# Performance work log

Hardware: AMD Instinct MI355X
Metric: run time of the kernel (lower is better)

## Reference

```python
import jax, jax.numpy as jnp
import numpy as np

H = 2        # num_heads
C = 128      # in_channels
K_ORDER = 4
BETA = 0.5


def _gcn_conv(x, row, col, deg_inv, n):
    # x: [N, H, C]; adj_t = D^{-1} A^T where A[row, col] = 1
    # (adj_t @ x)[c] = deg_inv[c] * sum_{e: col_e == c} x[row_e]
    msg = x[row]  # [E, H, C]
    agg = jax.ops.segment_sum(msg, col, num_segments=n)  # [N, H, C]
    return agg * deg_inv[:, None, None]


def _attn_conv(qs, ks, vs):
    # linear (kernelized) attention, non-block path
    n = qs.shape[0]
    kvs = jnp.einsum('lhm,lhd->hmd', ks, vs)            # [H, C, C]
    qkvs = jnp.einsum('nhm,hmd->nhd', qs, kvs)          # [N, H, C]
    vs_sum = vs.sum(axis=0)                             # [H, C]
    num = qkvs + vs_sum[None, :, :]
    ks_sum = ks.sum(axis=0)                             # [H, C]
    qks_sum = jnp.einsum('nhm,hm->nh', qs, ks_sum)[:, :, None]  # [N, H, 1]
    den = qks_sum + jnp.asarray(n, qs.dtype)
    return num / den


def setup_inputs() -> dict:
    key = jax.random.key(0)
    ks = jax.random.split(key, 8)
    N, E = 100000, 1600000
    x = jax.random.normal(ks[0], (N, C), jnp.float32)
    edge_index = jax.random.randint(ks[1], (2, E), 0, N, jnp.int64)
    s_in = 1.0 / np.sqrt(C)
    s_out = 1.0 / np.sqrt(H * C * (K_ORDER + 1))
    Wq_w = jax.random.normal(ks[2], (C, H * C), jnp.float32) * s_in
    Wq_b = jax.random.normal(ks[3], (H * C,), jnp.float32) * s_in
    Wk_w = jax.random.normal(ks[4], (C, H * C), jnp.float32) * s_in
    Wk_b = jax.random.normal(ks[5], (H * C,), jnp.float32) * s_in
    Wo_w = jax.random.normal(ks[6], (H * C * (K_ORDER + 1), C), jnp.float32) * s_out
    Wo_b = jax.random.normal(ks[7], (C,), jnp.float32) * s_out
    return {"x": x, "edge_index": edge_index, "Wq_w": Wq_w, "Wq_b": Wq_b,
            "Wk_w": Wk_w, "Wk_b": Wk_b, "Wo_w": Wo_w, "Wo_b": Wo_b}


def reference(x, edge_index, Wq_w, Wq_b, Wk_w, Wk_b, Wo_w, Wo_b):
    n = x.shape[0]
    row, col = edge_index[0], edge_index[1]
    # normalized adjacency D^{-1} A^T (pow(-1.0) in the source, not -0.5)
    deg = jax.ops.segment_sum(jnp.ones(row.shape[0], x.dtype), col, num_segments=n)
    deg_inv = jnp.where(deg > 0, 1.0 / deg, 0.0)

    query = (x @ Wq_w + Wq_b).reshape(n, H, C)
    key = (x @ Wk_w + Wk_b).reshape(n, H, C)
    qs = query / jnp.linalg.norm(query, axis=2, keepdims=True)
    ks = key / jnp.linalg.norm(key, axis=2, keepdims=True)

    x0 = jnp.broadcast_to(x[:, None, :], (n, H, C))  # [N, H, C]
    terms = [x0]
    for _ in range(K_ORDER):
        prev = terms[-1]
        gcn_i = _gcn_conv(prev, row, col, deg_inv, n)
        attn_i = _attn_conv(qs, ks, prev)
        terms.append(BETA * gcn_i + attn_i)
    xcat = jnp.concatenate(terms, axis=-1)  # [N, H, C*(K+1)]
    xcat = xcat.reshape(n, H * C * (K_ORDER + 1))
    return (xcat @ Wo_w + Wo_b) / H
```

## Files before the change

### kernel.cpp

```cpp
#include <hip/hip_runtime.h>

#define THREADS 256
#define NB 512
#define SEGCAP 6144

typedef __attribute__((ext_vector_type(8))) short short8;
typedef __attribute__((ext_vector_type(4))) float f32x4;

__device__ __forceinline__ float bf2f(unsigned short u) {
    union { unsigned int i; float f; } v;
    v.i = ((unsigned int)u) << 16;
    return v.f;
}
__device__ __forceinline__ unsigned short f2bf(float f) {
    union { float f; unsigned int i; } v;
    v.f = f;
    unsigned int r = (v.i + 0x7FFFu + ((v.i >> 16) & 1u)) >> 16;
    return (unsigned short)r;
}
__device__ __forceinline__ float4 ld4f(const float* p) {
    return *reinterpret_cast<const float4*>(p);
}
__device__ __forceinline__ float4 ld4f(const unsigned short* p) {
    ushort4 u = *reinterpret_cast<const ushort4*>(p);
    return make_float4(bf2f(u.x), bf2f(u.y), bf2f(u.z), bf2f(u.w));
}

__device__ __forceinline__ int edge_get(const int* base, int E, int mode, int which, int e) {
    size_t idx = (size_t)which * (size_t)E + (size_t)e;
    return mode ? base[2 * idx] : base[idx];
}

__global__ __launch_bounds__(256) void k_detect(const int* __restrict__ e, int E,
                                                int* __restrict__ mode) {
    __shared__ int nz;
    if (threadIdx.x == 0) nz = 0;
    __syncthreads();
    int lim = 2 * E;
    if (lim > 8192) lim = 8192;
    for (int i = 1 + 2 * (int)threadIdx.x; i < lim; i += 512)
        if (e[i] != 0) nz = 1;
    __syncthreads();
    if (threadIdx.x == 0) *mode = (nz == 0) ? 1 : 0;
}

__global__ __launch_bounds__(256) void k_hist(const int* __restrict__ eb, int E,
                                              const int* __restrict__ mode, int N, int CW, int epb,
                                              int* __restrict__ gcnt) {
    __shared__ int hist[NB];
    for (int i = threadIdx.x; i < NB; i += 256) hist[i] = 0;
    __syncthreads();
    int m = *mode;
    int e0 = blockIdx.x * epb;
    int e1 = min(e0 + epb, E);
    for (int e = e0 + threadIdx.x; e < e1; e += 256) {
        int c = edge_get(eb, E, m, 1, e);
        if ((unsigned)c < (unsigned)N) atomicAdd(&hist[c / CW], 1);
    }
    __syncthreads();
    for (int i = threadIdx.x; i < NB; i += 256)
        if (hist[i]) atomicAdd(&gcnt[i], hist[i]);
}

__global__ __launch_bounds__(NB) void k_bscan(const int* __restrict__ gcnt,
                                              int* __restrict__ gbase, int* __restrict__ gcursor) {
    __shared__ int s[NB];
    int t = threadIdx.x;
    int v = gcnt[t];
    s[t] = v;
    __syncthreads();
    for (int off = 1; off < NB; off <<= 1) {
        int add = (t >= off) ? s[t - off] : 0;
        __syncthreads();
        s[t] += add;
        __syncthreads();
    }
    gbase[t] = s[t] - v;
    gcursor[t] = s[t] - v;
}

__global__ __launch_bounds__(256) void k_part(const int* __restrict__ eb, int E,
                                              const int* __restrict__ mode, int N, int CW, int epb,
                                              int* __restrict__ gcursor, uint2* __restrict__ ebuf) {
    __shared__ int hist[NB];
    __shared__ int base[NB];
    for (int i = threadIdx.x; i < NB; i += 256) hist[i] = 0;
    __syncthreads();
    int m = *mode;
    int e0 = blockIdx.x * epb;
    int e1 = min(e0 + epb, E);
    for (int e = e0 + threadIdx.x; e < e1; e += 256) {
        int c = edge_get(eb, E, m, 1, e);
        if ((unsigned)c < (unsigned)N) atomicAdd(&hist[c / CW], 1);
    }
    __syncthreads();
    for (int i = threadIdx.x; i < NB; i += 256) {
        int h = hist[i];
        base[i] = h ? atomicAdd(&gcursor[i], h) : 0;
        hist[i] = 0;
    }
    __syncthreads();
    for (int e = e0 + threadIdx.x; e < e1; e += 256) {
        int c = edge_get(eb, E, m, 1, e);
        if ((unsigned)c < (unsigned)N) {
            int r = edge_get(eb, E, m, 0, e);
            if ((unsigned)r >= (unsigned)N) r = 0;
            int b = c / CW;
            int li = atomicAdd(&hist[b], 1);
            ebuf[(size_t)base[b] + li] = make_uint2((unsigned)r, (unsigned)c);
        }
    }
}

__global__ __launch_bounds__(256) void k_build(const uint2* __restrict__ ebuf,
                                               const int* __restrict__ gbase,
                                               const int* __restrict__ gcnt, int N, int CW,
                                               int* __restrict__ cnt, int* __restrict__ offs,
                                               float* __restrict__ deg_inv, int* __restrict__ csr) {
    __shared__ int hist[256];
    __shared__ int pfx[256];
    __shared__ int seg[SEGCAP];
    const int b = blockIdx.x;
    const int col0 = b * CW;
    const int ncols = min(CW, N - col0);
    if (ncols <= 0) return;
    const int ebase = gbase[b], ecnt = gcnt[b];
    const int t = threadIdx.x;
    for (int i = t; i < 256; i += 256) hist[i] = 0;
    __syncthreads();
    for (int e = t; e < ecnt; e += 256) {
        uint2 rc = ebuf[(size_t)ebase + e];
        atomicAdd(&hist[rc.y - col0], 1);
    }
    __syncthreads();
    int v = (t < ncols) ? hist[t] : 0;
    pfx[t] = v;
    __syncthreads();
    for (int off = 1; off < 256; off <<= 1) {
        int add = (t >= off) ? pfx[t - off] : 0;
        __syncthreads();
        pfx[t] += add;
        __syncthreads();
    }
    int excl = pfx[t] - v;
    if (t < ncols) {
        cnt[col0 + t] = v;
        offs[col0 + t] = ebase + excl;
        deg_inv[col0 + t] = (v > 0) ? 1.0f / (float)v : 0.0f;
    }
    __syncthreads();
    if (t < 256) hist[t] = (t < ncols) ? excl : 0;
    __syncthreads();
    if (ecnt <= SEGCAP) {
        for (int e = t; e < ecnt; e += 256) {
            uint2 rc = ebuf[(size_t)ebase + e];
            int li = atomicAdd(&hist[rc.y - col0], 1);
            seg[li] = (int)rc.x;
        }
        __syncthreads();
        for (int e = t; e < ecnt; e += 256) csr[(size_t)ebase + e] = seg[e];
    } else {
        for (int e = t; e < ecnt; e += 256) {
            uint2 rc = ebuf[(size_t)ebase + e];
            int li = atomicAdd(&hist[rc.y - col0], 1);
            csr[(size_t)ebase + li] = (int)rc.x;
        }
    }
}

__global__ __launch_bounds__(256) void k_prep_wqk(const float* __restrict__ Wq,
                                                  const float* __restrict__ Wk,
                                                  unsigned short* __restrict__ WqkT) {
    int i = blockIdx.x * 256 + threadIdx.x;
    if (i < 512 * 128) {
        int oc = i >> 7, k = i & 127;
        float v = (oc < 256) ? Wq[k * 256 + oc] : Wk[k * 256 + (oc - 256)];
        WqkT[i] = f2bf(v);
    }
}

__global__ __launch_bounds__(256) void k_prep_wo(const float* __restrict__ Wo,
                                                 unsigned short* __restrict__ WoT) {
    int i = blockIdx.x * 256 + threadIdx.x;
    if (i < 1280 * 128) {
        int r = i >> 7, j = i & 127;
        WoT[(size_t)j * 1280 + r] = f2bf(Wo[i]);
    }
}

__global__ __launch_bounds__(256) void k_proj(const float* __restrict__ x,
                                              const unsigned short* __restrict__ WqkT,
                                              const float* __restrict__ bq,
                                              const float* __restrict__ bk,
                                              unsigned short* __restrict__ qs,
                                              unsigned short* __restrict__ ks, int N) {
    __shared__ unsigned short xs[64 * 128];
    __shared__ unsigned short os[64 * 256];
    const int t = threadIdx.x;
    const int n0 = blockIdx.x * 64;
#pragma unroll
    for (int i = 0; i < 4; i++) {
        int chunk = i * 256 + t;
        int r = chunk >> 4, c0 = (chunk & 15) * 8;
        float4 a0 = make_float4(0.f, 0.f, 0.f, 0.f), a1 = a0;
        if (n0 + r < N) {
            a0 = ld4f(&x[(size_t)(n0 + r) * 128 + c0]);
            a1 = ld4f(&x[(size_t)(n0 + r) * 128 + c0 + 4]);
        }
        short8 v = {(short)f2bf(a0.x), (short)f2bf(a0.y), (short)f2bf(a0.z), (short)f2bf(a0.w),
                    (short)f2bf(a1.x), (short)f2bf(a1.y), (short)f2bf(a1.z), (short)f2bf(a1.w)};
        int byte = r * 256 + ((c0 * 2) ^ ((r & 7) << 4));
        *reinterpret_cast<short8*>(reinterpret_cast<char*>(xs) + byte) = v;
    }
    __syncthreads();
    const int w = t >> 6, l = t & 63, lrow = l & 15, lhi = l >> 4;
    f32x4 acc[4][8];
    const f32x4 fz = {0.f, 0.f, 0.f, 0.f};
#pragma unroll
    for (int mt = 0; mt < 4; mt++)
#pragma unroll
        for (int nt = 0; nt < 8; nt++) acc[mt][nt] = fz;

    for (int kk = 0; kk < 4; kk++) {
        int kb = kk * 32 + lhi * 8;
        short8 af[4];
#pragma unroll
        for (int mt = 0; mt < 4; mt++) {
            int r = mt * 16 + lrow;
            af[mt] = *reinterpret_cast<const short8*>(
                reinterpret_cast<const char*>(xs) + r * 256 + ((kb * 2) ^ ((r & 7) << 4)));
        }
#pragma unroll
        for (int nt = 0; nt < 8; nt++) {
            int oc = w * 128 + nt * 16 + lrow;
            short8 bf = *reinterpret_cast<const short8*>(&WqkT[(size_t)oc * 128 + kb]);
#pragma unroll
            for (int mt = 0; mt < 4; mt++)
                acc[mt][nt] = __builtin_amdgcn_mfma_f32_16x16x32_bf16(af[mt], bf, acc[mt][nt], 0, 0, 0);
        }
    }
#pragma unroll
    for (int nt = 0; nt < 8; nt++) {
        int oc = w * 128 + nt * 16 + lrow;
        float b = (oc < 256) ? bq[oc] : bk[oc - 256];
#pragma unroll
        for (int mt = 0; mt < 4; mt++)
#pragma unroll
            for (int reg = 0; reg < 4; reg++) acc[mt][nt][reg] += b;
    }
    const int hc = (w & 1) * 128;
    float rv[4][4];
#pragma unroll
    for (int mt = 0; mt < 4; mt++) {
        float ss[4] = {0.f, 0.f, 0.f, 0.f};
#pragma unroll
        for (int nt = 0; nt < 8; nt++)
#pragma unroll
            for (int reg = 0; reg < 4; reg++) ss[reg] += acc[mt][nt][reg] * acc[mt][nt][reg];
#pragma unroll
        for (int m_ = 1; m_ < 16; m_ <<= 1)
#pragma unroll
            for (int reg = 0; reg < 4; reg++) ss[reg] += __shfl_xor(ss[reg], m_);
#pragma unroll
        for (int reg = 0; reg < 4; reg++) rv[mt][reg] = rsqrtf(ss[reg]);
    }
    for (int pass = 0; pass < 2; pass++) {
        if ((w >> 1) == pass) {
#pragma unroll
            for (int mt = 0; mt < 4; mt++)
#pragma unroll
                for (int reg = 0; reg < 4; reg++) {
                    int r = mt * 16 + lhi * 4 + reg;
#pragma unroll
                    for (int nt = 0; nt < 8; nt++)
                        os[r * 256 + hc + nt * 16 + lrow] = f2bf(acc[mt][nt][reg] * rv[mt][reg]);
                }
        }
        __syncthreads();
        unsigned short* dstg = pass ? ks : qs;
#pragma unroll
        for (int i = 0; i < 8; i++) {
            int chunk = i * 256 + t;
            int r = chunk >> 5, c = (chunk & 31) * 8;
            int n = n0 + r;
            if (n < N)
                *reinterpret_cast<short8*>(&dstg[(size_t)n * 256 + c]) =
                    *reinterpret_cast<const short8*>(&os[r * 256 + c]);
        }
        __syncthreads();
    }
}

__global__ __launch_bounds__(256) void k_colsum(const unsigned short* __restrict__ ks, int N,
                                                float* __restrict__ part) {
    const int t = threadIdx.x;
    const int stride = (N + 255) >> 8;
    int r0 = blockIdx.x * stride;
    int rend = min(r0 + stride, N);
    float s = 0.f;
    for (int n = r0; n < rend; n++) s += bf2f(ks[(size_t)n * 256 + t]);
    part[blockIdx.x * 256 + t] = s;
}

__global__ __launch_bounds__(256) void k_colsum2(const float* __restrict__ part,
                                                 float* __restrict__ ks_sum) {
    const int t = threadIdx.x;
    float s = 0.f;
    for (int b = 0; b < 256; b++) s += part[b * 256 + t];
    ks_sum[t] = s;
}

__global__ __launch_bounds__(256) void k_den(const unsigned short* __restrict__ qs,
                                             const float* __restrict__ ks_sum,
                                             float* __restrict__ den, int N) {
    int w = threadIdx.x >> 6, lane = threadIdx.x & 63;
    int n = blockIdx.x * 4 + w;
    if (n >= N) return;
    float4 q = ld4f(&qs[(size_t)n * 256 + lane * 4]);
    float4 kv = *reinterpret_cast<const float4*>(&ks_sum[lane * 4]);
    float s = q.x * kv.x + q.y * kv.y + q.z * kv.z + q.w * kv.w;
#pragma unroll
    for (int off = 1; off < 32; off <<= 1) s += __shfl_xor(s, off);
    if ((lane & 31) == 0) den[n * 2 + (lane >> 5)] = s + (float)N;
}

__device__ __forceinline__ short8 frag_ld(const unsigned short* tile, int kb, int col) {
    const char* b = reinterpret_cast<const char*>(tile);
    int cb = (col * 2) ^ (((kb >> 3) & 3) << 5);
    short8 r;
#pragma unroll
    for (int i = 0; i < 8; i++)
        r[i] = (short)*reinterpret_cast<const unsigned short*>(b + (kb + i) * 512 + cb);
    return r;
}

template <typename TV>
__global__ __launch_bounds__(256) void k_kvs2(const unsigned short* __restrict__ ks,
                                              const TV* __restrict__ vs, int vstride, int vmask,
                                              float* __restrict__ partial,
                                              float* __restrict__ pvsum, int rows_per, int N) {
    __shared__ unsigned short kt[32 * 256];
    __shared__ unsigned short vt[32 * 256];
    __shared__ float vred[8][256];
    const int t = threadIdx.x;
    const int w = t >> 6, l = t & 63, lrow = l & 15, lhi = l >> 4;
    const int h = w >> 1, mhalf = w & 1;
    const int r0 = blockIdx.x * rows_per;
    const int rend = min(r0 + rows_per, N);

    const f32x4 fz = {0.f, 0.f, 0.f, 0.f};
    f32x4 acc[4][8];
#pragma unroll
    for (int mt = 0; mt < 4; mt++)
#pragma unroll
        for (int nt = 0; nt < 8; nt++) acc[mt][nt] = fz;
    float vsum8[8] = {0.f, 0.f, 0.f, 0.f, 0.f, 0.f, 0.f, 0.f};

    for (int c0 = r0; c0 < rend; c0 += 32) {
#pragma unroll
        for (int i = 0; i < 4; i++) {
            int chunk = i * 256 + t;
            int n = chunk >> 5, cc = (chunk & 31) * 8;
            short8 v = {0, 0, 0, 0, 0, 0, 0, 0};
            if (c0 + n < rend)
                v = *reinterpret_cast<const short8*>(&ks[(size_t)(c0 + n) * 256 + cc]);
            *reinterpret_cast<short8*>(reinterpret_cast<char*>(kt) + n * 512 +
                                       ((cc * 2) ^ (((n >> 3) & 3) << 5))) = v;
        }
#pragma unroll
        for (int i = 0; i < 4; i++) {
            int chunk = i * 256 + t;
            int n = chunk >> 5, cc = (chunk & 31) * 8;
            float4 a0 = make_float4(0.f, 0.f, 0.f, 0.f), a1 = a0;
            if (c0 + n < rend) {
                a0 = ld4f(&vs[(size_t)(c0 + n) * vstride + (cc & vmask)]);
                a1 = ld4f(&vs[(size_t)(c0 + n) * vstride + ((cc + 4) & vmask)]);
            }
            unsigned short u0 = f2bf(a0.x), u1 = f2bf(a0.y), u2 = f2bf(a0.z), u3 = f2bf(a0.w);
            unsigned short u4 = f2bf(a1.x), u5 = f2bf(a1.y), u6 = f2bf(a1.z), u7 = f2bf(a1.w);
            vsum8[0] += bf2f(u0); vsum8[1] += bf2f(u1); vsum8[2] += bf2f(u2); vsum8[3] += bf2f(u3);
            vsum8[4] += bf2f(u4); vsum8[5] += bf2f(u5); vsum8[6] += bf2f(u6); vsum8[7] += bf2f(u7);
            short8 v = {(short)u0, (short)u1, (short)u2, (short)u3,
                        (short)u4, (short)u5, (short)u6, (short)u7};
            *reinterpret_cast<short8*>(reinterpret_cast<char*>(vt) + n * 512 +
                                       ((cc * 2) ^ (((n >> 3) & 3) << 5))) = v;
        }
        __syncthreads();
        {
            int kb = lhi * 8;
            short8 af[4];
#pragma unroll
            for (int mt = 0; mt < 4; mt++)
                af[mt] = frag_ld(vt, kb, h * 128 + mhalf * 64 + mt * 16 + lrow);
#pragma unroll
            for (int nt = 0; nt < 8; nt++) {
                short8 bf = frag_ld(kt, kb, h * 128 + nt * 16 + lrow);
#pragma unroll
                for (int mt = 0; mt < 4; mt++)
                    acc[mt][nt] =
                        __builtin_amdgcn_mfma_f32_16x16x32_bf16(af[mt], bf, acc[mt][nt], 0, 0, 0);
            }
        }
        __syncthreads();
    }
    float* pb = &partial[((size_t)blockIdx.x * 2 + h) * 16384];
#pragma unroll
    for (int mt = 0; mt < 4; mt++)
#pragma unroll
        for (int reg = 0; reg < 4; reg++) {
            int c_local = mhalf * 64 + mt * 16 + lhi * 4 + reg;
#pragma unroll
            for (int nt = 0; nt < 8; nt++) pb[c_local * 128 + nt * 16 + lrow] = acc[mt][nt][reg];
        }
    {
        int cc = (t & 31) * 8;
#pragma unroll
        for (int j = 0; j < 8; j++) vred[t >> 5][cc + j] = vsum8[j];
        __syncthreads();
        float s = 0.f;
#pragma unroll
        for (int r = 0; r < 8; r++) s += vred[r][t];
        pvsum[blockIdx.x * 256 + t] = s;
    }
}

__global__ __launch_bounds__(256) void k_kvred(const float* __restrict__ partial,
                                               const float* __restrict__ pvsum, int S,
                                               unsigned short* __restrict__ kvsT,
                                               float* __restrict__ vs_sum) {
    if (blockIdx.x == 128) {
        int c = threadIdx.x;
        float s = 0.f;
        for (int i = 0; i < S; i++) s += pvsum[i * 256 + c];
        vs_sum[c] = s;
        return;
    }
    int e = blockIdx.x * 256 + threadIdx.x;
    float s = 0.f;
    for (int i = 0; i < S; i++) s += partial[(size_t)i * 32768 + e];
    kvsT[e] = f2bf(s);
}

__global__ __launch_bounds__(256) void k_gather2(const unsigned short* __restrict__ prev,
                                                 const int* __restrict__ csr_src,
                                                 const int* __restrict__ offs,
                                                 const int* __restrict__ cnt,
                                                 const float* __restrict__ deg_inv,
                                                 unsigned short* __restrict__ cur, int N) {
    const int w = threadIdx.x >> 6, l = threadIdx.x & 63;
    int n = blockIdx.x * 4 + w;
    if (n >= N) return;
    const int start = offs[n], d = cnt[n];
    int e = start;
    const int eend = start + d;
    float a0 = 0.f, a1 = 0.f, a2 = 0.f, a3 = 0.f;
    const int co = l * 4;
    for (; e + 8 <= eend; e += 8) {
        int s[8];
#pragma unroll
        for (int i = 0; i < 8; i++) s[i] = csr_src[e + i];
        ushort4 u[8];
#pragma unroll
        for (int i = 0; i < 8; i++)
            u[i] = *reinterpret_cast<const ushort4*>(&prev[(size_t)s[i] * 256 + co]);
#pragma unroll
        for (int i = 0; i < 8; i++) {
            a0 += bf2f(u[i].x); a1 += bf2f(u[i].y); a2 += bf2f(u[i].z); a3 += bf2f(u[i].w);
        }
    }
    for (; e < eend; e++) {
        ushort4 u = *reinterpret_cast<const ushort4*>(&prev[(size_t)csr_src[e] * 256 + co]);
        a0 += bf2f(u.x); a1 += bf2f(u.y); a2 += bf2f(u.z); a3 += bf2f(u.w);
    }
    float sc = 0.5f * deg_inv[n];
    ushort4 o;
    o.x = f2bf(a0 * sc); o.y = f2bf(a1 * sc); o.z = f2bf(a2 * sc); o.w = f2bf(a3 * sc);
    *reinterpret_cast<ushort4*>(&cur[(size_t)n * 256 + co]) = o;
}

__global__ __launch_bounds__(256) void k_gather2f(const float* __restrict__ prev,
                                                  const int* __restrict__ csr_src,
                                                  const int* __restrict__ offs,
                                                  const int* __restrict__ cnt,
                                                  const float* __restrict__ deg_inv,
                                                  unsigned short* __restrict__ cur, int N) {
    const int w = threadIdx.x >> 6, l = threadIdx.x & 63;
    int n = blockIdx.x * 4 + w;
    if (n >= N) return;
    const int start = offs[n], d = cnt[n];
    int e = start;
    const int eend = start + d;
    float a0 = 0.f, a1 = 0.f;
    const int co = l * 2;
    for (; e + 8 <= eend; e += 8) {
        int s[8];
#pragma unroll
        for (int i = 0; i < 8; i++) s[i] = csr_src[e + i];
        float2 u[8];
#pragma unroll
        for (int i = 0; i < 8; i++)
            u[i] = *reinterpret_cast<const float2*>(&prev[(size_t)s[i] * 128 + co]);
#pragma unroll
        for (int i = 0; i < 8; i++) { a0 += u[i].x; a1 += u[i].y; }
    }
    for (; e < eend; e++) {
        float2 u = *reinterpret_cast<const float2*>(&prev[(size_t)csr_src[e] * 128 + co]);
        a0 += u.x; a1 += u.y;
    }
    float sc = 0.5f * deg_inv[n];
    ushort2 o;
    o.x = f2bf(a0 * sc); o.y = f2bf(a1 * sc);
    *reinterpret_cast<ushort2*>(&cur[(size_t)n * 256 + co]) = o;
    *reinterpret_cast<ushort2*>(&cur[(size_t)n * 256 + 128 + co]) = o;
}

__global__ __launch_bounds__(256) void k_att_out(const unsigned short* __restrict__ qs,
                                                 const unsigned short* __restrict__ kvsT,
                                                 const float* __restrict__ vs_sum,
                                                 const float* __restrict__ den,
                                                 unsigned short* __restrict__ cur,
                                                 const unsigned short* __restrict__ WoT,
                                                 float* __restrict__ out, int tblk, int N) {
    __shared__ unsigned short sm[64 * 256];
    const int t = threadIdx.x;
    const int n0 = blockIdx.x * 64;
#pragma unroll
    for (int i = 0; i < 8; i++) {
        int chunk = i * 256 + t;
        int r = chunk >> 5, c0 = (chunk & 31) * 8;
        short8 v = {0, 0, 0, 0, 0, 0, 0, 0};
        if (n0 + r < N) v = *reinterpret_cast<const short8*>(&qs[(size_t)(n0 + r) * 256 + c0]);
        *reinterpret_cast<short8*>(reinterpret_cast<char*>(sm) + r * 512 +
                                   ((c0 * 2) ^ ((r & 7) << 4))) = v;
    }
    __syncthreads();
    const int w = t >> 6, l = t & 63, lrow = l & 15, lhi = l >> 4;
    const int h = w >> 1, jh = w & 1;
    const f32x4 fz = {0.f, 0.f, 0.f, 0.f};
    f32x4 acc[4][4];
#pragma unroll
    for (int mt = 0; mt < 4; mt++)
#pragma unroll
        for (int nt = 0; nt < 4; nt++) acc[mt][nt] = fz;

    for (int kk = 0; kk < 4; kk++) {
        int kb = kk * 32 + lhi * 8;
        short8 af[4];
#pragma unroll
        for (int mt = 0; mt < 4; mt++) {
            int r = mt * 16 + lrow;
            af[mt] = *reinterpret_cast<const short8*>(
                reinterpret_cast<const char*>(sm) + r * 512 +
                (((h * 128 + kb) * 2) ^ ((r & 7) << 4)));
        }
#pragma unroll
        for (int nt = 0; nt < 4; nt++) {
            int c = jh * 64 + nt * 16 + lrow;
            short8 bf = *reinterpret_cast<const short8*>(&kvsT[((size_t)h * 128 + c) * 128 + kb]);
#pragma unroll
            for (int mt = 0; mt < 4; mt++)
                acc[mt][nt] = __builtin_amdgcn_mfma_f32_16x16x32_bf16(af[mt], bf, acc[mt][nt], 0, 0, 0);
        }
    }
    __syncthreads();
#pragma unroll
    for (int i = 0; i < 8; i++) {
        int chunk = i * 256 + t;
        int r = chunk >> 5, c0 = (chunk & 31) * 8;
        short8 v = {0, 0, 0, 0, 0, 0, 0, 0};
        if (n0 + r < N) v = *reinterpret_cast<const short8*>(&cur[(size_t)(n0 + r) * 256 + c0]);
        *reinterpret_cast<short8*>(reinterpret_cast<char*>(sm) + r * 512 +
                                   ((c0 * 2) ^ ((r & 7) << 4))) = v;
    }
    __syncthreads();
#pragma unroll
    for (int mt = 0; mt < 4; mt++) {
#pragma unroll
        for (int reg = 0; reg < 4; reg++) {
            int r = mt * 16 + lhi * 4 + reg;
            int n = n0 + r;
            if (n < N) {
                float idn = 1.0f / den[n * 2 + h];
#pragma unroll
                for (int nt = 0; nt < 4; nt++) {
                    int c = h * 128 + jh * 64 + nt * 16 + lrow;
                    unsigned short* sp = reinterpret_cast<unsigned short*>(
                        reinterpret_cast<char*>(sm) + r * 512 + ((c * 2) ^ ((r & 7) << 4)));
                    float v = bf2f(*sp) + (acc[mt][nt][reg] + vs_sum[c]) * idn;
                    *sp = f2bf(v);
                }
            }
        }
    }
    __syncthreads();
#pragma unroll
    for (int i = 0; i < 8; i++) {
        int chunk = i * 256 + t;
        int r = chunk >> 5, c0 = (chunk & 31) * 8;
        int n = n0 + r;
        if (n < N)
            *reinterpret_cast<short8*>(&cur[(size_t)n * 256 + c0]) =
                *reinterpret_cast<const short8*>(reinterpret_cast<const char*>(sm) + r * 512 +
                                                 ((c0 * 2) ^ ((r & 7) << 4)));
    }
    __syncthreads();
    f32x4 acc2[4][2];
#pragma unroll
    for (int mt = 0; mt < 4; mt++)
#pragma unroll
        for (int nt = 0; nt < 2; nt++) acc2[mt][nt] = fz;
    for (int kk = 0; kk < 8; kk++) {
        int kb = kk * 32 + lhi * 8;
        short8 af[4];
#pragma unroll
        for (int mt = 0; mt < 4; mt++) {
            int r = mt * 16 + lrow;
            af[mt] = *reinterpret_cast<const short8*>(
                reinterpret_cast<const char*>(sm) + r * 512 + ((kb * 2) ^ ((r & 7) << 4)));
        }
        int woff = (kb >> 7) * 640 + tblk * 128 + (kb & 127);
#pragma unroll
        for (int nt = 0; nt < 2; nt++) {
            int j = w * 32 + nt * 16 + lrow;
            short8 bf = *reinterpret_cast<const short8*>(&WoT[(size_t)j * 1280 + woff]);
#pragma unroll
            for (int mt = 0; mt < 4; mt++)
                acc2[mt][nt] = __builtin_amdgcn_mfma_f32_16x16x32_bf16(af[mt], bf, acc2[mt][nt], 0, 0, 0);
        }
    }
#pragma unroll
    for (int nt = 0; nt < 2; nt++) {
        int j = w * 32 + nt * 16 + lrow;
#pragma unroll
        for (int mt = 0; mt < 4; mt++)
#pragma unroll
            for (int reg = 0; reg < 4; reg++) {
                int n = n0 + mt * 16 + lhi * 4 + reg;
                if (n < N) out[(size_t)n * 128 + j] += 0.5f * acc2[mt][nt][reg];
            }
    }
}

__global__ __launch_bounds__(256) void k_out0(const float* __restrict__ x,
                                              const unsigned short* __restrict__ WoT,
                                              const float* __restrict__ Wo_b,
                                              float* __restrict__ out, int N) {
    __shared__ unsigned short sm[64 * 256];
    const int t = threadIdx.x;
    const int n0 = blockIdx.x * 64;
#pragma unroll
    for (int i = 0; i < 8; i++) {
        int chunk = i * 256 + t;
        int r = chunk >> 5, c0 = (chunk & 31) * 8, cs = c0 & 127;
        float4 a0 = make_float4(0.f, 0.f, 0.f, 0.f), a1 = a0;
        if (n0 + r < N) {
            a0 = ld4f(&x[(size_t)(n0 + r) * 128 + cs]);
            a1 = ld4f(&x[(size_t)(n0 + r) * 128 + cs + 4]);
        }
        short8 v = {(short)f2bf(a0.x), (short)f2bf(a0.y), (short)f2bf(a0.z), (short)f2bf(a0.w),
                    (short)f2bf(a1.x), (short)f2bf(a1.y), (short)f2bf(a1.z), (short)f2bf(a1.w)};
        *reinterpret_cast<short8*>(reinterpret_cast<char*>(sm) + r * 512 +
                                   ((c0 * 2) ^ ((r & 7) << 4))) = v;
    }
    __syncthreads();
    const int w = t >> 6, l = t & 63, lrow = l & 15, lhi = l >> 4;
    const f32x4 fz = {0.f, 0.f, 0.f, 0.f};
    f32x4 acc2[4][2];
#pragma unroll
    for (int mt = 0; mt < 4; mt++)
#pragma unroll
        for (int nt = 0; nt < 2; nt++) acc2[mt][nt] = fz;
    for (int kk = 0; kk < 8; kk++) {
        int kb = kk * 32 + lhi * 8;
        short8 af[4];
#pragma unroll
        for (int mt = 0; mt < 4; mt++) {
            int r = mt * 16 + lrow;
            af[mt] = *reinterpret_cast<const short8*>(
                reinterpret_cast<const char*>(sm) + r * 512 + ((kb * 2) ^ ((r & 7) << 4)));
        }
        int woff = (kb >> 7) * 640 + (kb & 127);
#pragma unroll
        for (int nt = 0; nt < 2; nt++) {
            int j = w * 32 + nt * 16 + lrow;
            short8 bf = *reinterpret_cast<const short8*>(&WoT[(size_t)j * 1280 + woff]);
#pragma unroll
            for (int mt = 0; mt < 4; mt++)
                acc2[mt][nt] = __builtin_amdgcn_mfma_f32_16x16x32_bf16(af[mt], bf, acc2[mt][nt], 0, 0, 0);
        }
    }
#pragma unroll
    for (int nt = 0; nt < 2; nt++) {
        int j = w * 32 + nt * 16 + lrow;
        float b = Wo_b[j];
#pragma unroll
        for (int mt = 0; mt < 4; mt++)
#pragma unroll
            for (int reg = 0; reg < 4; reg++) {
                int n = n0 + mt * 16 + lhi * 4 + reg;
                if (n < N) out[(size_t)n * 128 + j] = 0.5f * (acc2[mt][nt][reg] + b);
            }
    }
}

extern "C" void kernel_launch(void* const* d_in, const int* in_sizes, int n_in,
                              void* d_out, int out_size, void* d_ws, size_t ws_size,
                              hipStream_t stream) {
    const int N = in_sizes[0] / 128;
    const int E = in_sizes[1] / 2;
    const float* x = (const float*)d_in[0];
    const int* eraw = (const int*)d_in[1];
    const float* Wq_w = (const float*)d_in[2];
    const float* Wq_b = (const float*)d_in[3];
    const float* Wk_w = (const float*)d_in[4];
    const float* Wk_b = (const float*)d_in[5];
    const float* Wo_w = (const float*)d_in[6];
    const float* Wo_b = (const float*)d_in[7];
    float* out = (float*)d_out;

    char* p = (char*)d_ws;
    auto alloc = [&](size_t bytes) -> void* {
        void* r = (void*)p;
        p += (bytes + 255) & ~(size_t)255;
        return r;
    };
    unsigned short* qs = (unsigned short*)alloc((size_t)N * 256 * 2);
    unsigned short* ks = (unsigned short*)alloc((size_t)N * 256 * 2);
    unsigned short* bufA = (unsigned short*)alloc((size_t)N * 256 * 2);
    unsigned short* bufB = (unsigned short*)alloc((size_t)N * 256 * 2);
    float* deg_inv = (float*)alloc((size_t)N * 4);
    float* den = (float*)alloc((size_t)N * 2 * 4);
    float* ks_sum = (float*)alloc(256 * 4);
    float* vs_sum = (float*)alloc(256 * 4);
    float* colpart = (float*)alloc(256 * 256 * 4);
    unsigned short* WqkT = (unsigned short*)alloc(512 * 128 * 2);
    unsigned short* WoT = (unsigned short*)alloc(1280 * 128 * 2);
    unsigned short* kvsTb = (unsigned short*)alloc(32768 * 2);
    int* cnt = (int*)alloc((size_t)N * 4);
    int* offs = (int*)alloc((size_t)N * 4);
    int* gcnt = (int*)alloc(NB * 4);
    int* gbase = (int*)alloc(NB * 4);
    int* gcursor = (int*)alloc(NB * 4);
    int* mode = (int*)alloc(256);
    int* csr = (int*)alloc((size_t)E * 4);
    uint2* ebuf = (uint2*)alloc((size_t)E * 8);

    size_t used = (size_t)(p - (char*)d_ws);
    size_t rem = (ws_size > used + (1 << 20)) ? ws_size - used - (1 << 20) : 0;
    int S = (int)(rem / (32768 * 4 + 1024));
    if (S > 256) S = 256;
    if (S < 8) S = 8;
    float* partial = (float*)alloc((size_t)S * 32768 * 4);
    float* pvsum = (float*)alloc((size_t)S * 256 * 4);
    const int rows_per = (N + S - 1) / S;

    const int CW = (N + NB - 1) / NB;
    const int EBLK = 256;
    const int epb = (E + EBLK - 1) / EBLK;

    hipMemsetAsync(gcnt, 0, NB * 4, stream);

    k_detect<<<1, 256, 0, stream>>>(eraw, E, mode);
    k_hist<<<EBLK, 256, 0, stream>>>(eraw, E, mode, N, CW, epb, gcnt);
    k_bscan<<<1, NB, 0, stream>>>(gcnt, gbase, gcursor);
    k_part<<<EBLK, 256, 0, stream>>>(eraw, E, mode, N, CW, epb, gcursor, ebuf);
    k_build<<<NB, 256, 0, stream>>>(ebuf, gbase, gcnt, N, CW, cnt, offs, deg_inv, csr);

    k_prep_wqk<<<256, 256, 0, stream>>>(Wq_w, Wk_w, WqkT);
    k_prep_wo<<<640, 256, 0, stream>>>(Wo_w, WoT);

    const int nb64 = (N + 63) / 64;
    k_proj<<<nb64, 256, 0, stream>>>(x, WqkT, Wq_b, Wk_b, qs, ks, N);
    k_colsum<<<256, 256, 0, stream>>>(ks, N, colpart);
    k_colsum2<<<1, 256, 0, stream>>>(colpart, ks_sum);
    k_den<<<(N + 3) / 4, 256, 0, stream>>>(qs, ks_sum, den, N);
    k_out0<<<nb64, 256, 0, stream>>>(x, WoT, Wo_b, out, N);

    const int gb4 = (N + 3) / 4;

    k_kvs2<float><<<S, 256, 0, stream>>>(ks, x, 128, 127, partial, pvsum, rows_per, N);
    k_kvred<<<129, 256, 0, stream>>>(partial, pvsum, S, kvsTb, vs_sum);
    k_gather2f<<<gb4, 256, 0, stream>>>(x, csr, offs, cnt, deg_inv, bufA, N);
    k_att_out<<<nb64, 256, 0, stream>>>(qs, kvsTb, vs_sum, den, bufA, WoT, out, 1, N);

    unsigned short* prev = bufA;
    unsigned short* cur = bufB;
    for (int step = 2; step <= 4; step++) {
        k_kvs2<unsigned short><<<S, 256, 0, stream>>>(ks, prev, 256, 255, partial, pvsum, rows_per,
                                                      N);
        k_kvred<<<129, 256, 0, stream>>>(partial, pvsum, S, kvsTb, vs_sum);
        k_gather2<<<gb4, 256, 0, stream>>>(prev, csr, offs, cnt, deg_inv, cur, N);
        k_att_out<<<nb64, 256, 0, stream>>>(qs, kvsTb, vs_sum, den, cur, WoT, out, step, N);
        unsigned short* tmp = prev;
        prev = cur;
        cur = tmp;
    }
}
```

Measured before the change: 1.795 ms.

## Fuse GCN neighbor gather into attention/output kernel via shared memory

Merges the CSR gather kernel into the attention+output-projection kernel. Each wave gathers neighbor sums for 16 rows directly into the swizzled LDS tile instead of writing to global memory and re-reading it. This removes a global round trip and a kernel launch per step. In exchange, the gather runs with far fewer blocks and per-wave serial rows, which may reduce the memory-latency hiding that the irregular gather depends on.

New measurement: 2.305 ms. 1.28x slower.

```diff
diff --git a/kernel.cpp b/kernel.cpp
--- a/kernel.cpp
+++ b/kernel.cpp
@@ -441,86 +441,19 @@
     kvsT[e] = f2bf(s);
 }
 
-__global__ __launch_bounds__(256) void k_gather2(const unsigned short* __restrict__ prev,
-                                                 const int* __restrict__ csr_src,
-                                                 const int* __restrict__ offs,
-                                                 const int* __restrict__ cnt,
-                                                 const float* __restrict__ deg_inv,
-                                                 unsigned short* __restrict__ cur, int N) {
-    const int w = threadIdx.x >> 6, l = threadIdx.x & 63;
-    int n = blockIdx.x * 4 + w;
-    if (n >= N) return;
-    const int start = offs[n], d = cnt[n];
-    int e = start;
-    const int eend = start + d;
-    float a0 = 0.f, a1 = 0.f, a2 = 0.f, a3 = 0.f;
-    const int co = l * 4;
-    for (; e + 8 <= eend; e += 8) {
-        int s[8];
-#pragma unroll
-        for (int i = 0; i < 8; i++) s[i] = csr_src[e + i];
-        ushort4 u[8];
-#pragma unroll
-        for (int i = 0; i < 8; i++)
-            u[i] = *reinterpret_cast<const ushort4*>(&prev[(size_t)s[i] * 256 + co]);
-#pragma unroll
-        for (int i = 0; i < 8; i++) {
-            a0 += bf2f(u[i].x); a1 += bf2f(u[i].y); a2 += bf2f(u[i].z); a3 += bf2f(u[i].w);
-        }
-    }
-    for (; e < eend; e++) {
-        ushort4 u = *reinterpret_cast<const ushort4*>(&prev[(size_t)csr_src[e] * 256 + co]);
-        a0 += bf2f(u.x); a1 += bf2f(u.y); a2 += bf2f(u.z); a3 += bf2f(u.w);
-    }
-    float sc = 0.5f * deg_inv[n];
-    ushort4 o;
-    o.x = f2bf(a0 * sc); o.y = f2bf(a1 * sc); o.z = f2bf(a2 * sc); o.w = f2bf(a3 * sc);
-    *reinterpret_cast<ushort4*>(&cur[(size_t)n * 256 + co]) = o;
-}
-
-__global__ __launch_bounds__(256) void k_gather2f(const float* __restrict__ prev,
-                                                  const int* __restrict__ csr_src,
-                                                  const int* __restrict__ offs,
-                                                  const int* __restrict__ cnt,
-                                                  const float* __restrict__ deg_inv,
-                                                  unsigned short* __restrict__ cur, int N) {
-    const int w = threadIdx.x >> 6, l = threadIdx.x & 63;
-    int n = blockIdx.x * 4 + w;
-    if (n >= N) return;
-    const int start = offs[n], d = cnt[n];
-    int e = start;
-    const int eend = start + d;
-    float a0 = 0.f, a1 = 0.f;
-    const int co = l * 2;
-    for (; e + 8 <= eend; e += 8) {
-        int s[8];
-#pragma unroll
-        for (int i = 0; i < 8; i++) s[i] = csr_src[e + i];
-        float2 u[8];
-#pragma unroll
-        for (int i = 0; i < 8; i++)
-            u[i] = *reinterpret_cast<const float2*>(&prev[(size_t)s[i] * 128 + co]);
-#pragma unroll
-        for (int i = 0; i < 8; i++) { a0 += u[i].x; a1 += u[i].y; }
-    }
-    for (; e < eend; e++) {
-        float2 u = *reinterpret_cast<const float2*>(&prev[(size_t)csr_src[e] * 128 + co]);
-        a0 += u.x; a1 += u.y;
-    }
-    float sc = 0.5f * deg_inv[n];
-    ushort2 o;
-    o.x = f2bf(a0 * sc); o.y = f2bf(a1 * sc);
-    *reinterpret_cast<ushort2*>(&cur[(size_t)n * 256 + co]) = o;
-    *reinterpret_cast<ushort2*>(&cur[(size_t)n * 256 + 128 + co]) = o;
-}
-
-__global__ __launch_bounds__(256) void k_att_out(const unsigned short* __restrict__ qs,
-                                                 const unsigned short* __restrict__ kvsT,
-                                                 const float* __restrict__ vs_sum,
-                                                 const float* __restrict__ den,
-                                                 unsigned short* __restrict__ cur,
-                                                 const unsigned short* __restrict__ WoT,
-                                                 float* __restrict__ out, int tblk, int N) {
+template <typename TV>
+__global__ __launch_bounds__(256) void k_fused(const unsigned short* __restrict__ qs,
+                                               const unsigned short* __restrict__ kvsT,
+                                               const float* __restrict__ vs_sum,
+                                               const float* __restrict__ den,
+                                               const TV* __restrict__ prev,
+                                               const int* __restrict__ csr_src,
+                                               const int* __restrict__ offs,
+                                               const int* __restrict__ cnt,
+                                               const float* __restrict__ deg_inv,
+                                               unsigned short* __restrict__ cur,
+                                               const unsigned short* __restrict__ WoT,
+                                               float* __restrict__ out, int tblk, int N) {
     __shared__ unsigned short sm[64 * 256];
     const int t = threadIdx.x;
     const int n0 = blockIdx.x * 64;
@@ -563,14 +496,70 @@
         }
     }
     __syncthreads();
-#pragma unroll
-    for (int i = 0; i < 8; i++) {
-        int chunk = i * 256 + t;
-        int r = chunk >> 5, c0 = (chunk & 31) * 8;
-        short8 v = {0, 0, 0, 0, 0, 0, 0, 0};
-        if (n0 + r < N) v = *reinterpret_cast<const short8*>(&cur[(size_t)(n0 + r) * 256 + c0]);
-        *reinterpret_cast<short8*>(reinterpret_cast<char*>(sm) + r * 512 +
-                                   ((c0 * 2) ^ ((r & 7) << 4))) = v;
+    for (int i = 0; i < 16; i++) {
+        int r = (w << 4) + i;
+        int n = n0 + r;
+        char* dst = reinterpret_cast<char*>(sm) + r * 512;
+        const int swz = (r & 7) << 4;
+        if (n < N) {
+            const int start = offs[n];
+            int e = start;
+            const int eend = start + cnt[n];
+            if constexpr (sizeof(TV) == 2) {
+                const int co = l * 4;
+                float a0 = 0.f, a1 = 0.f, a2 = 0.f, a3 = 0.f;
+                for (; e + 8 <= eend; e += 8) {
+                    int s[8];
+#pragma unroll
+                    for (int k = 0; k < 8; k++) s[k] = csr_src[e + k];
+                    ushort4 u[8];
+#pragma unroll
+                    for (int k = 0; k < 8; k++)
+                        u[k] = *reinterpret_cast<const ushort4*>(&prev[(size_t)s[k] * 256 + co]);
+#pragma unroll
+                    for (int k = 0; k < 8; k++) {
+                        a0 += bf2f(u[k].x); a1 += bf2f(u[k].y);
+                        a2 += bf2f(u[k].z); a3 += bf2f(u[k].w);
+                    }
+                }
+                for (; e < eend; e++) {
+                    ushort4 u =
+                        *reinterpret_cast<const ushort4*>(&prev[(size_t)csr_src[e] * 256 + co]);
+                    a0 += bf2f(u.x); a1 += bf2f(u.y); a2 += bf2f(u.z); a3 += bf2f(u.w);
+                }
+                float sc = 0.5f * deg_inv[n];
+                ushort4 o;
+                o.x = f2bf(a0 * sc); o.y = f2bf(a1 * sc);
+                o.z = f2bf(a2 * sc); o.w = f2bf(a3 * sc);
+                *reinterpret_cast<ushort4*>(dst + ((8 * l) ^ swz)) = o;
+            } else {
+                const int co = l * 2;
+                float a0 = 0.f, a1 = 0.f;
+                for (; e + 8 <= eend; e += 8) {
+                    int s[8];
+#pragma unroll
+                    for (int k = 0; k < 8; k++) s[k] = csr_src[e + k];
+                    float2 u[8];
+#pragma unroll
+                    for (int k = 0; k < 8; k++)
+                        u[k] = *reinterpret_cast<const float2*>(&prev[(size_t)s[k] * 128 + co]);
+#pragma unroll
+                    for (int k = 0; k < 8; k++) { a0 += u[k].x; a1 += u[k].y; }
+                }
+                for (; e < eend; e++) {
+                    float2 u =
+                        *reinterpret_cast<const float2*>(&prev[(size_t)csr_src[e] * 128 + co]);
+                    a0 += u.x; a1 += u.y;
+                }
+                float sc = 0.5f * deg_inv[n];
+                ushort2 o;
+                o.x = f2bf(a0 * sc); o.y = f2bf(a1 * sc);
+                *reinterpret_cast<ushort2*>(dst + ((4 * l) ^ swz)) = o;
+                *reinterpret_cast<ushort2*>(dst + ((256 + 4 * l) ^ swz)) = o;
+            }
+        } else {
+            *reinterpret_cast<ushort4*>(dst + ((8 * l) ^ swz)) = make_ushort4(0, 0, 0, 0);
+        }
     }
     __syncthreads();
 #pragma unroll
@@ -603,7 +592,6 @@
                 *reinterpret_cast<const short8*>(reinterpret_cast<const char*>(sm) + r * 512 +
                                                  ((c0 * 2) ^ ((r & 7) << 4)));
     }
-    __syncthreads();
     f32x4 acc2[4][2];
 #pragma unroll
     for (int mt = 0; mt < 4; mt++)
@@ -776,12 +764,10 @@
     k_den<<<(N + 3) / 4, 256, 0, stream>>>(qs, ks_sum, den, N);
     k_out0<<<nb64, 256, 0, stream>>>(x, WoT, Wo_b, out, N);
 
-    const int gb4 = (N + 3) / 4;
-
     k_kvs2<float><<<S, 256, 0, stream>>>(ks, x, 128, 127, partial, pvsum, rows_per, N);
     k_kvred<<<129, 256, 0, stream>>>(partial, pvsum, S, kvsTb, vs_sum);
-    k_gather2f<<<gb4, 256, 0, stream>>>(x, csr, offs, cnt, deg_inv, bufA, N);
-    k_att_out<<<nb64, 256, 0, stream>>>(qs, kvsTb, vs_sum, den, bufA, WoT, out, 1, N);
+    k_fused<float><<<nb64, 256, 0, stream>>>(qs, kvsTb, vs_sum, den, x, csr, offs, cnt, deg_inv,
+                                             bufA, WoT, out, 1, N);
 
     unsigned short* prev = bufA;
     unsigned short* cur = bufB;
@@ -789,8 +775,8 @@
         k_kvs2<unsigned short><<<S, 256, 0, stream>>>(ks, prev, 256, 255, partial, pvsum, rows_per,
                                                       N);
         k_kvred<<<129, 256, 0, stream>>>(partial, pvsum, S, kvsTb, vs_sum);
-        k_gather2<<<gb4, 256, 0, stream>>>(prev, csr, offs, cnt, deg_inv, cur, N);
-        k_att_out<<<nb64, 256, 0, stream>>>(qs, kvsTb, vs_sum, den, cur, WoT, out, step, N);
+        k_fused<unsigned short><<<nb64, 256, 0, stream>>>(qs, kvsTb, vs_sum, den, prev, csr, offs,
+                                                          cnt, deg_inv, cur, WoT, out, step, N);
         unsigned short* tmp = prev;
         prev = cur;
         cur = tmp;
```
